# Performance work log

Hardware: AMD Instinct MI355X
Metric: run time of the kernel (lower is better)

The kernel has to match this reference:

```python
import jax, jax.numpy as jnp
import numpy as np

HIDDEN = 2048
KEY_DIM = 2048
NUM_HEADS = 16
EPS = 1e-05


def rms_norm(x, w, eps=EPS):
    ms = jnp.mean(x * x, axis=-1, keepdims=True)
    return x * jax.lax.rsqrt(ms + eps) * w


def setup_inputs() -> dict:
    key = jax.random.key(0)
    ks = jax.random.split(key, 6)
    bound = 1.0 / np.sqrt(HIDDEN)  # kaiming-uniform-ish scale
    x = jax.random.normal(ks[0], (2, 2048, HIDDEN), dtype=jnp.float32)
    rms_w = jnp.ones((HIDDEN,), dtype=jnp.float32)
    Wq = jax.random.uniform(ks[1], (HIDDEN, KEY_DIM), jnp.float32, -bound, bound)
    Wk = jax.random.uniform(ks[2], (HIDDEN, KEY_DIM), jnp.float32, -bound, bound)
    Wv = jax.random.uniform(ks[3], (HIDDEN, KEY_DIM), jnp.float32, -bound, bound)
    Wo = jax.random.uniform(ks[4], (KEY_DIM, HIDDEN), jnp.float32, -bound, bound)
    return {"x": x, "rms_w": rms_w, "Wq": Wq, "Wk": Wk, "Wv": Wv, "Wo": Wo}


def reference(x, rms_w, Wq, Wk, Wv, Wo):
    B, S, _ = x.shape
    residual = x
    xn = rms_norm(x, rms_w)
    # project and split heads: [B,S,H,Dh]
    q = (xn @ Wq).reshape(B, S, NUM_HEADS, KEY_DIM // NUM_HEADS)
    k = (xn @ Wk).reshape(B, S, NUM_HEADS, KEY_DIM // NUM_HEADS)
    v = (xn @ Wv).reshape(B, S, NUM_HEADS, KEY_DIM // NUM_HEADS)
    # NOTE: original scales by 1/sqrt(key_dim), not head_dim — kept faithful
    scale = 1.0 / jnp.sqrt(jnp.float32(KEY_DIM))
    scores = jnp.einsum('bshd,bthd->bhst', q, k) * scale  # [B,H,S,S]
    causal = jnp.tril(jnp.ones((S, S), dtype=bool))
    scores = jnp.where(causal[None, None], scores, -jnp.inf)
    probs = jax.nn.softmax(scores, axis=-1)  # stable max-subtract internally
    out = jnp.einsum('bhst,bthd->bshd', probs, v).reshape(B, S, KEY_DIM)
    return out @ Wo + residual
```

## Files before the change

### kernel.cpp

```cpp
#include <hip/hip_runtime.h>
#include <math.h>

typedef __attribute__((ext_vector_type(8))) short bf16x8;
typedef __attribute__((ext_vector_type(4))) float f32x4;
typedef __attribute__((ext_vector_type(16))) float f32x16;

#define HID 2048
#define SEQ 2048
#define NH  16
#define DH  128
#define QK_SCALE 0.02209708691207961f

__device__ __forceinline__ ushort f2bf(float f) {
  union { float f; unsigned u; } v; v.f = f;
  unsigned r = v.u + 0x7fffu + ((v.u >> 16) & 1u);
  return (ushort)(r >> 16);
}

__device__ __forceinline__ void gload16(const ushort* g, ushort* l) {
  __builtin_amdgcn_global_load_lds((const __attribute__((address_space(1))) void*)g,
                                   (__attribute__((address_space(3))) void*)l,
                                   16, 0, 0);
}

__global__ __launch_bounds__(256) void k_transpose(const float* __restrict__ W,
                                                   ushort* __restrict__ Wt) {
  __shared__ float t[32][33];
  int n0 = blockIdx.x * 32, k0 = blockIdx.y * 32;
  int tx = threadIdx.x, ty = threadIdx.y;
  for (int i = ty; i < 32; i += 8)
    t[i][tx] = W[(size_t)(k0 + i) * HID + n0 + tx];
  __syncthreads();
  for (int i = ty; i < 32; i += 8)
    Wt[(size_t)(n0 + i) * HID + k0 + tx] = f2bf(t[tx][i]);
}

__global__ __launch_bounds__(256) void k_rmsnorm(const float* __restrict__ x,
                                                 const float* __restrict__ w,
                                                 ushort* __restrict__ xn) {
  int row = blockIdx.x;
  const float* xr = x + (size_t)row * HID;
  int base = threadIdx.x * 8;
  float4 a = *(const float4*)(xr + base);
  float4 c = *(const float4*)(xr + base + 4);
  float ss = a.x*a.x + a.y*a.y + a.z*a.z + a.w*a.w
           + c.x*c.x + c.y*c.y + c.z*c.z + c.w*c.w;
  #pragma unroll
  for (int off = 32; off > 0; off >>= 1) ss += __shfl_xor(ss, off);
  __shared__ float red[4];
  if ((threadIdx.x & 63) == 0) red[threadIdx.x >> 6] = ss;
  __syncthreads();
  float tot = red[0] + red[1] + red[2] + red[3];
  float sc = rsqrtf(tot * (1.0f / HID) + 1e-5f);
  float4 wa = *(const float4*)(w + base);
  float4 wc = *(const float4*)(w + base + 4);
  ushort h[8];
  h[0] = f2bf(a.x * sc * wa.x); h[1] = f2bf(a.y * sc * wa.y);
  h[2] = f2bf(a.z * sc * wa.z); h[3] = f2bf(a.w * sc * wa.w);
  h[4] = f2bf(c.x * sc * wc.x); h[5] = f2bf(c.y * sc * wc.y);
  h[6] = f2bf(c.z * sc * wc.z); h[7] = f2bf(c.w * sc * wc.w);
  int4 pk;
  pk.x = h[0] | ((int)h[1] << 16);
  pk.y = h[2] | ((int)h[3] << 16);
  pk.z = h[4] | ((int)h[5] << 16);
  pk.w = h[6] | ((int)h[7] << 16);
  *(int4*)&xn[(size_t)row * HID + base] = pk;
}

template <int MODE>
__global__ __launch_bounds__(256) void k_gemm(const ushort* __restrict__ A,
                                              const ushort* __restrict__ Bt,
                                              ushort* __restrict__ obf,
                                              ushort* __restrict__ vt,
                                              float* __restrict__ ofl,
                                              const float* __restrict__ resid,
                                              int K) {
  __shared__ ushort sA[128 * 64];
  __shared__ ushort sB[128 * 64];
  const int tid = threadIdx.x;
  const int lane = tid & 63, w = tid >> 6;
  const int wr = w >> 1, wc = w & 1;
  const int bm = blockIdx.y, bn = blockIdx.x;
  const int g = lane >> 4, l15 = lane & 15;
  f32x4 zero = {0.f, 0.f, 0.f, 0.f};
  f32x4 acc[4][4];
  #pragma unroll
  for (int i = 0; i < 4; ++i)
    #pragma unroll
    for (int j = 0; j < 4; ++j) acc[i][j] = zero;

  for (int k0 = 0; k0 < K; k0 += 64) {
    #pragma unroll
    for (int c = 0; c < 4; ++c) {
      int id = (w * 4 + c) * 64 + lane;
      int r = id >> 3, ck = id & 7;
      int ke = k0 + ((ck ^ (r & 7)) * 8);
      gload16(&A[(size_t)(bm * 128 + r) * K + ke], ((ushort*)sA) + (size_t)(w * 4 + c) * 512);
      gload16(&Bt[(size_t)(bn * 128 + r) * K + ke], ((ushort*)sB) + (size_t)(w * 4 + c) * 512);
    }
    __syncthreads();
    #pragma unroll
    for (int kk = 0; kk < 2; ++kk) {
      bf16x8 aF[4], bF[4];
      #pragma unroll
      for (int i = 0; i < 4; ++i) {
        int row = wr * 64 + i * 16 + l15;
        int cp = (kk * 4 + g) ^ (lane & 7);
        aF[i] = *(const bf16x8*)&sA[row * 64 + cp * 8];
      }
      #pragma unroll
      for (int j = 0; j < 4; ++j) {
        int row = wc * 64 + j * 16 + l15;
        int cp = (kk * 4 + g) ^ (lane & 7);
        bF[j] = *(const bf16x8*)&sB[row * 64 + cp * 8];
      }
      #pragma unroll
      for (int i = 0; i < 4; ++i)
        #pragma unroll
        for (int j = 0; j < 4; ++j)
          acc[i][j] = __builtin_amdgcn_mfma_f32_16x16x32_bf16(aF[i], bF[j], acc[i][j], 0, 0, 0);
    }
    __syncthreads();
  }

  int rbase = bm * 128 + wr * 64 + (lane >> 4) * 4;
  int cbase = bn * 128 + wc * 64 + l15;
  #pragma unroll
  for (int i = 0; i < 4; ++i) {
    #pragma unroll
    for (int j = 0; j < 4; ++j) {
      int col = cbase + j * 16;
      #pragma unroll
      for (int r = 0; r < 4; ++r) {
        int row = rbase + i * 16 + r;
        float v = acc[i][j][r];
        if (MODE == 0) {
          ushort hv = f2bf(v);
          if (col < 4096) {
            obf[(size_t)row * 4096 + col] = hv;
          } else {
            int nv = col - 4096;
            int h = nv >> 7, d = nv & 127;
            int b = row >> 11, s = row & 2047;
            vt[(size_t)((b * NH + h) * DH + d) * SEQ + s] = hv;
          }
        } else {
          ofl[(size_t)row * HID + col] = v + resid[(size_t)row * HID + col];
        }
      }
    }
  }
}

__global__ __launch_bounds__(256, 2) void k_attn2(const ushort* __restrict__ qk,
                                                  const ushort* __restrict__ vt,
                                                  ushort* __restrict__ aout) {
  __shared__ ushort sK[64 * 128];
  __shared__ ushort sV[128 * 64];
  const int tid = threadIdx.x;
  const int lane = tid & 63, w = tid >> 6;
  const int h2 = lane >> 5;
  const int l31 = lane & 31;
  const int bid = blockIdx.x;
  const int t = bid >> 3;
  const int bh = (bid & 7) + 8 * (t >> 4);
  const int qblk = 15 - (t & 15);
  const int b = bh >> 4, hh = bh & 15;
  const int q0w = qblk * 128 + w * 32;

  bf16x8 qf[8];
  {
    const ushort* qbase = qk + (size_t)(b * SEQ + q0w + l31) * 4096 + hh * DH;
    #pragma unroll
    for (int kk = 0; kk < 8; ++kk) qf[kk] = *(const bf16x8*)&qbase[kk * 16 + h2 * 8];
  }

  f32x16 accO[4];
  #pragma unroll
  for (int i = 0; i < 4; ++i)
    #pragma unroll
    for (int r = 0; r < 16; ++r) accO[i][r] = 0.f;
  float m_r = -1e30f, l_r = 0.f;

  const int ntile = 2 * qblk + 2;
  for (int tt = 0; tt < ntile; ++tt) {
    const int t0 = tt * 64;
    #pragma unroll
    for (int c = 0; c < 4; ++c) {
      int id = (w * 4 + c) * 64 + lane;
      int kr = id >> 4, ck = id & 15;
      gload16(qk + (size_t)(b * SEQ + t0 + kr) * 4096 + 2048 + hh * DH + ((ck ^ (kr & 7)) * 8),
              ((ushort*)sK) + (size_t)(w * 4 + c) * 512);
      int dr = id >> 3, cv = id & 7;
      gload16(vt + (size_t)(bh * DH + dr) * SEQ + t0 + ((cv ^ (dr & 7)) * 8),
              ((ushort*)sV) + (size_t)(w * 4 + c) * 512);
    }
    __syncthreads();

    if (t0 <= q0w + 31) {
      f32x16 accS[2];
      #pragma unroll
      for (int i = 0; i < 2; ++i)
        #pragma unroll
        for (int r = 0; r < 16; ++r) accS[i][r] = 0.f;
      #pragma unroll
      for (int kt = 0; kt < 2; ++kt) {
        const int row = kt * 32 + l31;
        #pragma unroll
        for (int kk = 0; kk < 8; ++kk) {
          const int cp = (kk * 2 + h2) ^ (lane & 7);
          bf16x8 kf = *(const bf16x8*)&sK[row * 128 + cp * 8];
          accS[kt] = __builtin_amdgcn_mfma_f32_32x32x16_bf16(kf, qf[kk], accS[kt], 0, 0, 0);
        }
      }
      const int qa = q0w + l31;
      float pmax = -INFINITY;
      if (t0 + 63 <= q0w) {
        #pragma unroll
        for (int kt = 0; kt < 2; ++kt)
          #pragma unroll
          for (int r = 0; r < 16; ++r) {
            float s = accS[kt][r] * QK_SCALE;
            accS[kt][r] = s;
            pmax = fmaxf(pmax, s);
          }
      } else {
        #pragma unroll
        for (int kt = 0; kt < 2; ++kt)
          #pragma unroll
          for (int r = 0; r < 16; ++r) {
            int ka = t0 + kt * 32 + (r & 3) + 8 * (r >> 2) + 4 * h2;
            float s = (ka <= qa) ? accS[kt][r] * QK_SCALE : -INFINITY;
            accS[kt][r] = s;
            pmax = fmaxf(pmax, s);
          }
      }
      pmax = fmaxf(pmax, __shfl_xor(pmax, 32));
      if (__any(pmax > m_r + 8.f)) {
        float mn = fmaxf(m_r, pmax);
        float al = __expf(m_r - mn);
        m_r = mn;
        l_r *= al;
        #pragma unroll
        for (int r = 0; r < 16; ++r) {
          float ar = __shfl(al, (r & 3) + 8 * (r >> 2) + 4 * h2);
          #pragma unroll
          for (int ds = 0; ds < 4; ++ds) accO[ds][r] *= ar;
        }
      }
      float rs = 0.f;
      #pragma unroll
      for (int kt = 0; kt < 2; ++kt)
        #pragma unroll
        for (int r = 0; r < 16; ++r) {
          float p = __expf(accS[kt][r] - m_r);
          rs += p;
          accS[kt][r] = p;
        }
      rs += __shfl_xor(rs, 32);
      l_r += rs;
      uint W[2][4][2];
      #pragma unroll
      for (int kt = 0; kt < 2; ++kt)
        #pragma unroll
        for (int bq = 0; bq < 4; ++bq)
          #pragma unroll
          for (int w2 = 0; w2 < 2; ++w2) {
            uint u0 = __float_as_uint(accS[kt][bq * 4 + w2 * 2]);
            uint u1 = __float_as_uint(accS[kt][bq * 4 + w2 * 2 + 1]);
            W[kt][bq][w2] = (u0 >> 16) | (u1 & 0xffff0000u);
          }
      #pragma unroll
      for (int kc = 0; kc < 4; ++kc) {
        const int kt = kc >> 1, pq = kc & 1;
        uint X0 = W[kt][2 * pq][0],     X1 = W[kt][2 * pq][1];
        uint Y0 = W[kt][2 * pq + 1][0], Y1 = W[kt][2 * pq + 1][1];
        uint sx0 = (uint)__shfl_xor((int)X0, 32);
        uint sx1 = (uint)__shfl_xor((int)X1, 32);
        uint sy0 = (uint)__shfl_xor((int)Y0, 32);
        uint sy1 = (uint)__shfl_xor((int)Y1, 32);
        union { uint u[4]; bf16x8 v; } pu;
        pu.u[0] = h2 ? sy0 : X0;
        pu.u[1] = h2 ? sy1 : X1;
        pu.u[2] = h2 ? Y0 : sx0;
        pu.u[3] = h2 ? Y1 : sx1;
        #pragma unroll
        for (int ds = 0; ds < 4; ++ds) {
          const int dr = ds * 32 + l31;
          const int cp = (kc * 2 + h2) ^ (lane & 7);
          bf16x8 vf = *(const bf16x8*)&sV[dr * 64 + cp * 8];
          accO[ds] = __builtin_amdgcn_mfma_f32_32x32x16_bf16(pu.v, vf, accO[ds], 0, 0, 0);
        }
      }
    }
    __syncthreads();
  }

  float linv = 1.f / l_r;
  #pragma unroll
  for (int r = 0; r < 16; ++r) {
    int qrel = (r & 3) + 8 * (r >> 2) + 4 * h2;
    float li = __shfl(linv, qrel);
    #pragma unroll
    for (int ds = 0; ds < 4; ++ds) {
      aout[(size_t)(b * SEQ + q0w + qrel) * HID + hh * DH + ds * 32 + l31] =
          f2bf(accO[ds][r] * li);
    }
  }
}

extern "C" void kernel_launch(void* const* d_in, const int* in_sizes, int n_in,
                              void* d_out, int out_size, void* d_ws, size_t ws_size,
                              hipStream_t stream) {
  const float* x     = (const float*)d_in[0];
  const float* rms_w = (const float*)d_in[1];
  const float* Wq    = (const float*)d_in[2];
  const float* Wk    = (const float*)d_in[3];
  const float* Wv    = (const float*)d_in[4];
  const float* Wo    = (const float*)d_in[5];
  float* out = (float*)d_out;

  char* ws = (char*)d_ws;
  ushort* WqkvT = (ushort*)ws; ws += (size_t)6144 * 2048 * 2;
  ushort* WoT   = (ushort*)ws; ws += (size_t)2048 * 2048 * 2;
  ushort* xn    = (ushort*)ws; ws += (size_t)4096 * 2048 * 2;
  ushort* qkbuf = (ushort*)ws; ws += (size_t)4096 * 4096 * 2;
  ushort* vt    = (ushort*)ws; ws += (size_t)4096 * 2048 * 2;
  ushort* aout  = (ushort*)ws; ws += (size_t)4096 * 2048 * 2;

  dim3 tb(32, 8), tg(64, 64);
  k_transpose<<<tg, tb, 0, stream>>>(Wq, WqkvT);
  k_transpose<<<tg, tb, 0, stream>>>(Wk, WqkvT + (size_t)2048 * 2048);
  k_transpose<<<tg, tb, 0, stream>>>(Wv, WqkvT + (size_t)4096 * 2048);
  k_transpose<<<tg, tb, 0, stream>>>(Wo, WoT);

  k_rmsnorm<<<4096, 256, 0, stream>>>(x, rms_w, xn);

  k_gemm<0><<<dim3(48, 32), 256, 0, stream>>>(xn, WqkvT, qkbuf, vt, nullptr, nullptr, 2048);

  k_attn2<<<512, 256, 0, stream>>>(qkbuf, vt, aout);

  k_gemm<1><<<dim3(16, 32), 256, 0, stream>>>(aout, WoT, nullptr, nullptr, out, x, 2048);
}
```

Measured before the change: 302.0 us.

## Rewrite GEMM with 256x128 tiles, 4-stage async LDS pipeline and block swizzle

Replaces the single-buffered 128x128 GEMM with a 512-thread 256x128-tile kernel. It uses a 4-deep ring of LDS buffers filled by direct global-to-LDS loads, with vmcnt-based waits so loads overlap MFMA compute, and raises wave priority around the MFMA block. Block indices are swizzled so that consecutive blocks share operand tiles, aimed at better cache reuse. The changes are meant to hide global load latency and remove the double __syncthreads per k-step, at the cost of more LDS (96KB) and hand-tuned waitcnt logic that relies on exact load counts.

New measurement: 293.3 us. 1.03x faster.

```diff
diff --git a/kernel.cpp b/kernel.cpp
--- a/kernel.cpp
+++ b/kernel.cpp
@@ -68,63 +68,96 @@
 }
 
 template <int MODE>
-__global__ __launch_bounds__(256) void k_gemm(const ushort* __restrict__ A,
-                                              const ushort* __restrict__ Bt,
-                                              ushort* __restrict__ obf,
-                                              ushort* __restrict__ vt,
-                                              float* __restrict__ ofl,
-                                              const float* __restrict__ resid,
-                                              int K) {
-  __shared__ ushort sA[128 * 64];
-  __shared__ ushort sB[128 * 64];
+__global__ __launch_bounds__(512, 2) void k_gemm2(const ushort* __restrict__ A,
+                                                  const ushort* __restrict__ Bt,
+                                                  ushort* __restrict__ obf,
+                                                  ushort* __restrict__ vt,
+                                                  float* __restrict__ ofl,
+                                                  const float* __restrict__ resid) {
+  constexpr int K = 2048, NS = 64;
+  constexpr int NBN = (MODE == 0) ? 48 : 16;
+  constexpr int QX = ((MODE == 0) ? 768 : 256) / 8;
+  __shared__ ushort lds[4][12288];
   const int tid = threadIdx.x;
   const int lane = tid & 63, w = tid >> 6;
-  const int wr = w >> 1, wc = w & 1;
-  const int bm = blockIdx.y, bn = blockIdx.x;
+  const int wm = w >> 1, wn = w & 1;
   const int g = lane >> 4, l15 = lane & 15;
-  f32x4 zero = {0.f, 0.f, 0.f, 0.f};
+  const int swz = (blockIdx.x & 7) * QX + (blockIdx.x >> 3);
+  const int bm = swz / NBN, bn = swz % NBN;
+
   f32x4 acc[4][4];
   #pragma unroll
   for (int i = 0; i < 4; ++i)
     #pragma unroll
-    for (int j = 0; j < 4; ++j) acc[i][j] = zero;
-
-  for (int k0 = 0; k0 < K; k0 += 64) {
-    #pragma unroll
-    for (int c = 0; c < 4; ++c) {
-      int id = (w * 4 + c) * 64 + lane;
-      int r = id >> 3, ck = id & 7;
-      int ke = k0 + ((ck ^ (r & 7)) * 8);
-      gload16(&A[(size_t)(bm * 128 + r) * K + ke], ((ushort*)sA) + (size_t)(w * 4 + c) * 512);
-      gload16(&Bt[(size_t)(bn * 128 + r) * K + ke], ((ushort*)sB) + (size_t)(w * 4 + c) * 512);
-    }
-    __syncthreads();
-    #pragma unroll
-    for (int kk = 0; kk < 2; ++kk) {
-      bf16x8 aF[4], bF[4];
-      #pragma unroll
-      for (int i = 0; i < 4; ++i) {
-        int row = wr * 64 + i * 16 + l15;
-        int cp = (kk * 4 + g) ^ (lane & 7);
-        aF[i] = *(const bf16x8*)&sA[row * 64 + cp * 8];
-      }
-      #pragma unroll
-      for (int j = 0; j < 4; ++j) {
-        int row = wc * 64 + j * 16 + l15;
-        int cp = (kk * 4 + g) ^ (lane & 7);
-        bF[j] = *(const bf16x8*)&sB[row * 64 + cp * 8];
-      }
-      #pragma unroll
-      for (int i = 0; i < 4; ++i)
-        #pragma unroll
-        for (int j = 0; j < 4; ++j)
-          acc[i][j] = __builtin_amdgcn_mfma_f32_16x16x32_bf16(aF[i], bF[j], acc[i][j], 0, 0, 0);
-    }
-    __syncthreads();
-  }
-
-  int rbase = bm * 128 + wr * 64 + (lane >> 4) * 4;
-  int cbase = bn * 128 + wc * 64 + l15;
+    for (int j = 0; j < 4; ++j) acc[i][j] = f32x4{0.f, 0.f, 0.f, 0.f};
+
+  auto STAGE = [&](int s) {
+    const int ch = s & 3, k0 = s * 32;
+    #pragma unroll
+    for (int c = 0; c < 2; ++c) {
+      int idx = c * 512 + tid;
+      int r = idx >> 2, cp = idx & 3;
+      int ck = cp ^ ((r >> 1) & 3);
+      gload16(&A[(size_t)(bm * 256 + r) * K + k0 + ck * 8],
+              &lds[ch][(c * 8 + w) * 512]);
+    }
+    {
+      int r = tid >> 2, cp = tid & 3;
+      int ck = cp ^ ((r >> 1) & 3);
+      gload16(&Bt[(size_t)(bn * 128 + r) * K + k0 + ck * 8],
+              &lds[ch][8192 + w * 512]);
+    }
+  };
+
+  auto COMPUTE = [&](int s) {
+    const ushort* La = lds[s & 3];
+    const ushort* Lb = La + 8192;
+    bf16x8 aF[4], bF[4];
+    #pragma unroll
+    for (int i = 0; i < 4; ++i) {
+      int row = wm * 64 + i * 16 + l15;
+      int cp = g ^ ((row >> 1) & 3);
+      aF[i] = *(const bf16x8*)&La[row * 32 + cp * 8];
+    }
+    #pragma unroll
+    for (int j = 0; j < 4; ++j) {
+      int row = wn * 64 + j * 16 + l15;
+      int cp = g ^ ((row >> 1) & 3);
+      bF[j] = *(const bf16x8*)&Lb[row * 32 + cp * 8];
+    }
+    __builtin_amdgcn_s_setprio(1);
+    #pragma unroll
+    for (int i = 0; i < 4; ++i)
+      #pragma unroll
+      for (int j = 0; j < 4; ++j)
+        acc[i][j] = __builtin_amdgcn_mfma_f32_16x16x32_bf16(aF[i], bF[j], acc[i][j], 0, 0, 0);
+    __builtin_amdgcn_s_setprio(0);
+  };
+
+  STAGE(0); STAGE(1); STAGE(2);
+  #pragma unroll 1
+  for (int s = 0; s <= NS - 4; ++s) {
+    asm volatile("s_waitcnt vmcnt(6)" ::: "memory");
+    __builtin_amdgcn_s_barrier();
+    __builtin_amdgcn_sched_barrier(0);
+    STAGE(s + 3);
+    COMPUTE(s);
+  }
+  asm volatile("s_waitcnt vmcnt(6)" ::: "memory");
+  __builtin_amdgcn_s_barrier();
+  __builtin_amdgcn_sched_barrier(0);
+  COMPUTE(NS - 3);
+  asm volatile("s_waitcnt vmcnt(3)" ::: "memory");
+  __builtin_amdgcn_s_barrier();
+  __builtin_amdgcn_sched_barrier(0);
+  COMPUTE(NS - 2);
+  asm volatile("s_waitcnt vmcnt(0)" ::: "memory");
+  __builtin_amdgcn_s_barrier();
+  __builtin_amdgcn_sched_barrier(0);
+  COMPUTE(NS - 1);
+
+  int rbase = bm * 256 + wm * 64 + g * 4;
+  int cbase = bn * 128 + wn * 64 + l15;
   #pragma unroll
   for (int i = 0; i < 4; ++i) {
     #pragma unroll
@@ -336,9 +369,9 @@
 
   k_rmsnorm<<<4096, 256, 0, stream>>>(x, rms_w, xn);
 
-  k_gemm<0><<<dim3(48, 32), 256, 0, stream>>>(xn, WqkvT, qkbuf, vt, nullptr, nullptr, 2048);
+  k_gemm2<0><<<768, 512, 0, stream>>>(xn, WqkvT, qkbuf, vt, nullptr, nullptr);
 
   k_attn2<<<512, 256, 0, stream>>>(qkbuf, vt, aout);
 
-  k_gemm<1><<<dim3(16, 32), 256, 0, stream>>>(aout, WoT, nullptr, nullptr, out, x, 2048);
-}
+  k_gemm2<1><<<256, 512, 0, stream>>>(aout, WoT, nullptr, nullptr, out, x);
+}
```

## Double-buffer LDS in GEMM and attention loops, merge weight transposes into one launch

Applied to the files above, without the earlier changes.

The GEMM and attention kernels now double-buffer their shared-memory tiles and prefetch the next tile with async global-to-LDS loads while computing the current one. Explicit vmcnt waits and raw barriers replace __syncthreads, so memory latency can overlap MFMA work. The four weight-transpose launches are merged into one 3D-grid launch. Shared memory per block doubles, which may lower occupancy, especially for the attention kernel with its launch bound of 2 blocks.

Measured after the change: 301.8 us. Within noise of the previous version (-0.1%).

```diff
diff --git a/kernel.cpp b/kernel.cpp
--- a/kernel.cpp
+++ b/kernel.cpp
@@ -23,9 +23,19 @@
                                    16, 0, 0);
 }
 
-__global__ __launch_bounds__(256) void k_transpose(const float* __restrict__ W,
-                                                   ushort* __restrict__ Wt) {
+#define VMCNT(n) asm volatile("s_waitcnt vmcnt(" #n ")" ::: "memory")
+#define BAR()    __builtin_amdgcn_s_barrier()
+
+__global__ __launch_bounds__(256) void k_transpose4(const float* __restrict__ W0,
+                                                    const float* __restrict__ W1,
+                                                    const float* __restrict__ W2,
+                                                    const float* __restrict__ W3,
+                                                    ushort* __restrict__ T0,
+                                                    ushort* __restrict__ T3) {
   __shared__ float t[32][33];
+  int z = blockIdx.z;
+  const float* W = (z == 0) ? W0 : (z == 1) ? W1 : (z == 2) ? W2 : W3;
+  ushort* Wt = (z == 3) ? T3 : (T0 + (size_t)z * 2048 * 2048);
   int n0 = blockIdx.x * 32, k0 = blockIdx.y * 32;
   int tx = threadIdx.x, ty = threadIdx.y;
   for (int i = ty; i < 32; i += 8)
@@ -68,37 +78,38 @@
 }
 
 template <int MODE>
-__global__ __launch_bounds__(256) void k_gemm(const ushort* __restrict__ A,
-                                              const ushort* __restrict__ Bt,
-                                              ushort* __restrict__ obf,
-                                              ushort* __restrict__ vt,
-                                              float* __restrict__ ofl,
-                                              const float* __restrict__ resid,
-                                              int K) {
-  __shared__ ushort sA[128 * 64];
-  __shared__ ushort sB[128 * 64];
+__global__ __launch_bounds__(256) void k_gemm4(const ushort* __restrict__ A,
+                                               const ushort* __restrict__ Bt,
+                                               ushort* __restrict__ obf,
+                                               ushort* __restrict__ vt,
+                                               float* __restrict__ ofl,
+                                               const float* __restrict__ resid,
+                                               int K) {
+  __shared__ ushort sA[2][128 * 64];
+  __shared__ ushort sB[2][128 * 64];
   const int tid = threadIdx.x;
   const int lane = tid & 63, w = tid >> 6;
   const int wr = w >> 1, wc = w & 1;
   const int bm = blockIdx.y, bn = blockIdx.x;
   const int g = lane >> 4, l15 = lane & 15;
-  f32x4 zero = {0.f, 0.f, 0.f, 0.f};
   f32x4 acc[4][4];
   #pragma unroll
   for (int i = 0; i < 4; ++i)
     #pragma unroll
-    for (int j = 0; j < 4; ++j) acc[i][j] = zero;
-
-  for (int k0 = 0; k0 < K; k0 += 64) {
+    for (int j = 0; j < 4; ++j) acc[i][j] = f32x4{0.f, 0.f, 0.f, 0.f};
+
+  auto STAGE = [&](int t, int buf) {
+    const int k0 = t * 64;
     #pragma unroll
     for (int c = 0; c < 4; ++c) {
       int id = (w * 4 + c) * 64 + lane;
       int r = id >> 3, ck = id & 7;
       int ke = k0 + ((ck ^ (r & 7)) * 8);
-      gload16(&A[(size_t)(bm * 128 + r) * K + ke], ((ushort*)sA) + (size_t)(w * 4 + c) * 512);
-      gload16(&Bt[(size_t)(bn * 128 + r) * K + ke], ((ushort*)sB) + (size_t)(w * 4 + c) * 512);
-    }
-    __syncthreads();
+      gload16(&A[(size_t)(bm * 128 + r) * K + ke], &sA[buf][(w * 4 + c) * 512]);
+      gload16(&Bt[(size_t)(bn * 128 + r) * K + ke], &sB[buf][(w * 4 + c) * 512]);
+    }
+  };
+  auto COMPUTE = [&](int buf) {
     #pragma unroll
     for (int kk = 0; kk < 2; ++kk) {
       bf16x8 aF[4], bF[4];
@@ -106,13 +117,13 @@
       for (int i = 0; i < 4; ++i) {
         int row = wr * 64 + i * 16 + l15;
         int cp = (kk * 4 + g) ^ (lane & 7);
-        aF[i] = *(const bf16x8*)&sA[row * 64 + cp * 8];
+        aF[i] = *(const bf16x8*)&sA[buf][row * 64 + cp * 8];
       }
       #pragma unroll
       for (int j = 0; j < 4; ++j) {
         int row = wc * 64 + j * 16 + l15;
         int cp = (kk * 4 + g) ^ (lane & 7);
-        bF[j] = *(const bf16x8*)&sB[row * 64 + cp * 8];
+        bF[j] = *(const bf16x8*)&sB[buf][row * 64 + cp * 8];
       }
       #pragma unroll
       for (int i = 0; i < 4; ++i)
@@ -120,10 +131,23 @@
         for (int j = 0; j < 4; ++j)
           acc[i][j] = __builtin_amdgcn_mfma_f32_16x16x32_bf16(aF[i], bF[j], acc[i][j], 0, 0, 0);
     }
-    __syncthreads();
-  }
-
-  int rbase = bm * 128 + wr * 64 + (lane >> 4) * 4;
+  };
+
+  const int nt = K / 64;
+  STAGE(0, 0);
+  #pragma unroll 1
+  for (int t = 0; t < nt - 1; ++t) {
+    STAGE(t + 1, (t + 1) & 1);
+    VMCNT(8);
+    BAR();
+    COMPUTE(t & 1);
+    BAR();
+  }
+  VMCNT(0);
+  BAR();
+  COMPUTE((nt - 1) & 1);
+
+  int rbase = bm * 128 + wr * 64 + g * 4;
   int cbase = bn * 128 + wc * 64 + l15;
   #pragma unroll
   for (int i = 0; i < 4; ++i) {
@@ -152,11 +176,11 @@
   }
 }
 
-__global__ __launch_bounds__(256, 2) void k_attn2(const ushort* __restrict__ qk,
+__global__ __launch_bounds__(256, 2) void k_attn3(const ushort* __restrict__ qk,
                                                   const ushort* __restrict__ vt,
                                                   ushort* __restrict__ aout) {
-  __shared__ ushort sK[64 * 128];
-  __shared__ ushort sV[128 * 64];
+  __shared__ ushort sK[2][64 * 128];
+  __shared__ ushort sV[2][128 * 64];
   const int tid = threadIdx.x;
   const int lane = tid & 63, w = tid >> 6;
   const int h2 = lane >> 5;
@@ -182,119 +206,131 @@
     for (int r = 0; r < 16; ++r) accO[i][r] = 0.f;
   float m_r = -1e30f, l_r = 0.f;
 
-  const int ntile = 2 * qblk + 2;
-  for (int tt = 0; tt < ntile; ++tt) {
+  auto STAGE = [&](int tt, int buf) {
     const int t0 = tt * 64;
     #pragma unroll
     for (int c = 0; c < 4; ++c) {
       int id = (w * 4 + c) * 64 + lane;
       int kr = id >> 4, ck = id & 15;
       gload16(qk + (size_t)(b * SEQ + t0 + kr) * 4096 + 2048 + hh * DH + ((ck ^ (kr & 7)) * 8),
-              ((ushort*)sK) + (size_t)(w * 4 + c) * 512);
+              &sK[buf][(size_t)(w * 4 + c) * 512]);
       int dr = id >> 3, cv = id & 7;
       gload16(vt + (size_t)(bh * DH + dr) * SEQ + t0 + ((cv ^ (dr & 7)) * 8),
-              ((ushort*)sV) + (size_t)(w * 4 + c) * 512);
-    }
-    __syncthreads();
-
-    if (t0 <= q0w + 31) {
-      f32x16 accS[2];
-      #pragma unroll
-      for (int i = 0; i < 2; ++i)
-        #pragma unroll
-        for (int r = 0; r < 16; ++r) accS[i][r] = 0.f;
-      #pragma unroll
-      for (int kt = 0; kt < 2; ++kt) {
-        const int row = kt * 32 + l31;
-        #pragma unroll
-        for (int kk = 0; kk < 8; ++kk) {
-          const int cp = (kk * 2 + h2) ^ (lane & 7);
-          bf16x8 kf = *(const bf16x8*)&sK[row * 128 + cp * 8];
-          accS[kt] = __builtin_amdgcn_mfma_f32_32x32x16_bf16(kf, qf[kk], accS[kt], 0, 0, 0);
+              &sV[buf][(size_t)(w * 4 + c) * 512]);
+    }
+  };
+
+  auto COMPUTE = [&](int tt, int buf) {
+    const int t0 = tt * 64;
+    f32x16 accS[2];
+    #pragma unroll
+    for (int i = 0; i < 2; ++i)
+      #pragma unroll
+      for (int r = 0; r < 16; ++r) accS[i][r] = 0.f;
+    #pragma unroll
+    for (int kt = 0; kt < 2; ++kt) {
+      const int row = kt * 32 + l31;
+      #pragma unroll
+      for (int kk = 0; kk < 8; ++kk) {
+        const int cp = (kk * 2 + h2) ^ (lane & 7);
+        bf16x8 kf = *(const bf16x8*)&sK[buf][row * 128 + cp * 8];
+        accS[kt] = __builtin_amdgcn_mfma_f32_32x32x16_bf16(kf, qf[kk], accS[kt], 0, 0, 0);
+      }
+    }
+    const int qa = q0w + l31;
+    float pmax = -INFINITY;
+    if (t0 + 63 <= q0w) {
+      #pragma unroll
+      for (int kt = 0; kt < 2; ++kt)
+        #pragma unroll
+        for (int r = 0; r < 16; ++r) {
+          float s = accS[kt][r] * QK_SCALE;
+          accS[kt][r] = s;
+          pmax = fmaxf(pmax, s);
         }
-      }
-      const int qa = q0w + l31;
-      float pmax = -INFINITY;
-      if (t0 + 63 <= q0w) {
-        #pragma unroll
-        for (int kt = 0; kt < 2; ++kt)
-          #pragma unroll
-          for (int r = 0; r < 16; ++r) {
-            float s = accS[kt][r] * QK_SCALE;
-            accS[kt][r] = s;
-            pmax = fmaxf(pmax, s);
-          }
-      } else {
-        #pragma unroll
-        for (int kt = 0; kt < 2; ++kt)
-          #pragma unroll
-          for (int r = 0; r < 16; ++r) {
-            int ka = t0 + kt * 32 + (r & 3) + 8 * (r >> 2) + 4 * h2;
-            float s = (ka <= qa) ? accS[kt][r] * QK_SCALE : -INFINITY;
-            accS[kt][r] = s;
-            pmax = fmaxf(pmax, s);
-          }
-      }
-      pmax = fmaxf(pmax, __shfl_xor(pmax, 32));
-      if (__any(pmax > m_r + 8.f)) {
-        float mn = fmaxf(m_r, pmax);
-        float al = __expf(m_r - mn);
-        m_r = mn;
-        l_r *= al;
+    } else {
+      #pragma unroll
+      for (int kt = 0; kt < 2; ++kt)
         #pragma unroll
         for (int r = 0; r < 16; ++r) {
-          float ar = __shfl(al, (r & 3) + 8 * (r >> 2) + 4 * h2);
-          #pragma unroll
-          for (int ds = 0; ds < 4; ++ds) accO[ds][r] *= ar;
+          int ka = t0 + kt * 32 + (r & 3) + 8 * (r >> 2) + 4 * h2;
+          float s = (ka <= qa) ? accS[kt][r] * QK_SCALE : -INFINITY;
+          accS[kt][r] = s;
+          pmax = fmaxf(pmax, s);
         }
-      }
-      float rs = 0.f;
-      #pragma unroll
-      for (int kt = 0; kt < 2; ++kt)
-        #pragma unroll
-        for (int r = 0; r < 16; ++r) {
-          float p = __expf(accS[kt][r] - m_r);
-          rs += p;
-          accS[kt][r] = p;
+    }
+    pmax = fmaxf(pmax, __shfl_xor(pmax, 32));
+    if (__any(pmax > m_r + 8.f)) {
+      float mn = fmaxf(m_r, pmax);
+      float al = __expf(m_r - mn);
+      m_r = mn;
+      l_r *= al;
+      #pragma unroll
+      for (int r = 0; r < 16; ++r) {
+        float ar = __shfl(al, (r & 3) + 8 * (r >> 2) + 4 * h2);
+        #pragma unroll
+        for (int ds = 0; ds < 4; ++ds) accO[ds][r] *= ar;
+      }
+    }
+    float rs = 0.f;
+    #pragma unroll
+    for (int kt = 0; kt < 2; ++kt)
+      #pragma unroll
+      for (int r = 0; r < 16; ++r) {
+        float p = __expf(accS[kt][r] - m_r);
+        rs += p;
+        accS[kt][r] = p;
+      }
+    rs += __shfl_xor(rs, 32);
+    l_r += rs;
+    uint W[2][4][2];
+    #pragma unroll
+    for (int kt = 0; kt < 2; ++kt)
+      #pragma unroll
+      for (int bq = 0; bq < 4; ++bq)
+        #pragma unroll
+        for (int w2 = 0; w2 < 2; ++w2) {
+          uint u0 = __float_as_uint(accS[kt][bq * 4 + w2 * 2]);
+          uint u1 = __float_as_uint(accS[kt][bq * 4 + w2 * 2 + 1]);
+          W[kt][bq][w2] = (u0 >> 16) | (u1 & 0xffff0000u);
         }
-      rs += __shfl_xor(rs, 32);
-      l_r += rs;
-      uint W[2][4][2];
-      #pragma unroll
-      for (int kt = 0; kt < 2; ++kt)
-        #pragma unroll
-        for (int bq = 0; bq < 4; ++bq)
-          #pragma unroll
-          for (int w2 = 0; w2 < 2; ++w2) {
-            uint u0 = __float_as_uint(accS[kt][bq * 4 + w2 * 2]);
-            uint u1 = __float_as_uint(accS[kt][bq * 4 + w2 * 2 + 1]);
-            W[kt][bq][w2] = (u0 >> 16) | (u1 & 0xffff0000u);
-          }
-      #pragma unroll
-      for (int kc = 0; kc < 4; ++kc) {
-        const int kt = kc >> 1, pq = kc & 1;
-        uint X0 = W[kt][2 * pq][0],     X1 = W[kt][2 * pq][1];
-        uint Y0 = W[kt][2 * pq + 1][0], Y1 = W[kt][2 * pq + 1][1];
-        uint sx0 = (uint)__shfl_xor((int)X0, 32);
-        uint sx1 = (uint)__shfl_xor((int)X1, 32);
-        uint sy0 = (uint)__shfl_xor((int)Y0, 32);
-        uint sy1 = (uint)__shfl_xor((int)Y1, 32);
-        union { uint u[4]; bf16x8 v; } pu;
-        pu.u[0] = h2 ? sy0 : X0;
-        pu.u[1] = h2 ? sy1 : X1;
-        pu.u[2] = h2 ? Y0 : sx0;
-        pu.u[3] = h2 ? Y1 : sx1;
-        #pragma unroll
-        for (int ds = 0; ds < 4; ++ds) {
-          const int dr = ds * 32 + l31;
-          const int cp = (kc * 2 + h2) ^ (lane & 7);
-          bf16x8 vf = *(const bf16x8*)&sV[dr * 64 + cp * 8];
-          accO[ds] = __builtin_amdgcn_mfma_f32_32x32x16_bf16(pu.v, vf, accO[ds], 0, 0, 0);
-        }
-      }
-    }
-    __syncthreads();
-  }
+    #pragma unroll
+    for (int kc = 0; kc < 4; ++kc) {
+      const int kt = kc >> 1, pq = kc & 1;
+      uint X0 = W[kt][2 * pq][0],     X1 = W[kt][2 * pq][1];
+      uint Y0 = W[kt][2 * pq + 1][0], Y1 = W[kt][2 * pq + 1][1];
+      uint sx0 = (uint)__shfl_xor((int)X0, 32);
+      uint sx1 = (uint)__shfl_xor((int)X1, 32);
+      uint sy0 = (uint)__shfl_xor((int)Y0, 32);
+      uint sy1 = (uint)__shfl_xor((int)Y1, 32);
+      union { uint u[4]; bf16x8 v; } pu;
+      pu.u[0] = h2 ? sy0 : X0;
+      pu.u[1] = h2 ? sy1 : X1;
+      pu.u[2] = h2 ? Y0 : sx0;
+      pu.u[3] = h2 ? Y1 : sx1;
+      #pragma unroll
+      for (int ds = 0; ds < 4; ++ds) {
+        const int dr = ds * 32 + l31;
+        const int cp = (kc * 2 + h2) ^ (lane & 7);
+        bf16x8 vf = *(const bf16x8*)&sV[buf][dr * 64 + cp * 8];
+        accO[ds] = __builtin_amdgcn_mfma_f32_32x32x16_bf16(pu.v, vf, accO[ds], 0, 0, 0);
+      }
+    }
+  };
+
+  const int ntile = 2 * qblk + 2;
+  STAGE(0, 0);
+  #pragma unroll 1
+  for (int tt = 0; tt < ntile - 1; ++tt) {
+    STAGE(tt + 1, (tt + 1) & 1);
+    VMCNT(8);
+    BAR();
+    if (tt * 64 <= q0w + 31) COMPUTE(tt, tt & 1);
+    BAR();
+  }
+  VMCNT(0);
+  BAR();
+  COMPUTE(ntile - 1, (ntile - 1) & 1);
 
   float linv = 1.f / l_r;
   #pragma unroll
@@ -328,17 +364,13 @@
   ushort* vt    = (ushort*)ws; ws += (size_t)4096 * 2048 * 2;
   ushort* aout  = (ushort*)ws; ws += (size_t)4096 * 2048 * 2;
 
-  dim3 tb(32, 8), tg(64, 64);
-  k_transpose<<<tg, tb, 0, stream>>>(Wq, WqkvT);
-  k_transpose<<<tg, tb, 0, stream>>>(Wk, WqkvT + (size_t)2048 * 2048);
-  k_transpose<<<tg, tb, 0, stream>>>(Wv, WqkvT + (size_t)4096 * 2048);
-  k_transpose<<<tg, tb, 0, stream>>>(Wo, WoT);
+  k_transpose4<<<dim3(64, 64, 4), dim3(32, 8), 0, stream>>>(Wq, Wk, Wv, Wo, WqkvT, WoT);
 
   k_rmsnorm<<<4096, 256, 0, stream>>>(x, rms_w, xn);
 
-  k_gemm<0><<<dim3(48, 32), 256, 0, stream>>>(xn, WqkvT, qkbuf, vt, nullptr, nullptr, 2048);
-
-  k_attn2<<<512, 256, 0, stream>>>(qkbuf, vt, aout);
-
-  k_gemm<1><<<dim3(16, 32), 256, 0, stream>>>(aout, WoT, nullptr, nullptr, out, x, 2048);
-}
+  k_gemm4<0><<<dim3(48, 32), 256, 0, stream>>>(xn, WqkvT, qkbuf, vt, nullptr, nullptr, 2048);
+
+  k_attn3<<<512, 256, 0, stream>>>(qkbuf, vt, aout);
+
+  k_gemm4<1><<<dim3(16, 32), 256, 0, stream>>>(aout, WoT, nullptr, nullptr, out, x, 2048);
+}
```

## Enlarge GEMM tiles to 256x128 and merge four weight transposes into one launch

Applied to the files above, without the earlier changes.

The GEMM block tile grows from 128x128 to 256x128, so each wave now computes a 128x64 sub-tile with 8x4 MFMA accumulators. This raises arithmetic intensity per LDS load and halves the number of blocks. The four separate weight-transpose launches are folded into a single 3D-grid launch to cut launch overhead. The cost is more registers per thread and more LDS per block. The output-projection GEMM shrinks to only 256 blocks, which may underfill the 256 CUs.

After: 311.0 us. 3.0% more time.

```diff
diff --git a/kernel.cpp b/kernel.cpp
--- a/kernel.cpp
+++ b/kernel.cpp
@@ -23,9 +23,16 @@
                                    16, 0, 0);
 }
 
-__global__ __launch_bounds__(256) void k_transpose(const float* __restrict__ W,
-                                                   ushort* __restrict__ Wt) {
+__global__ __launch_bounds__(256) void k_transpose4(const float* __restrict__ W0,
+                                                    const float* __restrict__ W1,
+                                                    const float* __restrict__ W2,
+                                                    const float* __restrict__ W3,
+                                                    ushort* __restrict__ T0,
+                                                    ushort* __restrict__ T3) {
   __shared__ float t[32][33];
+  int z = blockIdx.z;
+  const float* W = (z == 0) ? W0 : (z == 1) ? W1 : (z == 2) ? W2 : W3;
+  ushort* Wt = (z == 3) ? T3 : (T0 + (size_t)z * 2048 * 2048);
   int n0 = blockIdx.x * 32, k0 = blockIdx.y * 32;
   int tx = threadIdx.x, ty = threadIdx.y;
   for (int i = ty; i < 32; i += 8)
@@ -68,43 +75,48 @@
 }
 
 template <int MODE>
-__global__ __launch_bounds__(256) void k_gemm(const ushort* __restrict__ A,
-                                              const ushort* __restrict__ Bt,
-                                              ushort* __restrict__ obf,
-                                              ushort* __restrict__ vt,
-                                              float* __restrict__ ofl,
-                                              const float* __restrict__ resid,
-                                              int K) {
-  __shared__ ushort sA[128 * 64];
+__global__ __launch_bounds__(256, 2) void k_gemm6(const ushort* __restrict__ A,
+                                                  const ushort* __restrict__ Bt,
+                                                  ushort* __restrict__ obf,
+                                                  ushort* __restrict__ vt,
+                                                  float* __restrict__ ofl,
+                                                  const float* __restrict__ resid,
+                                                  int K) {
+  __shared__ ushort sA[256 * 64];
   __shared__ ushort sB[128 * 64];
   const int tid = threadIdx.x;
   const int lane = tid & 63, w = tid >> 6;
   const int wr = w >> 1, wc = w & 1;
   const int bm = blockIdx.y, bn = blockIdx.x;
   const int g = lane >> 4, l15 = lane & 15;
-  f32x4 zero = {0.f, 0.f, 0.f, 0.f};
-  f32x4 acc[4][4];
-  #pragma unroll
-  for (int i = 0; i < 4; ++i)
-    #pragma unroll
-    for (int j = 0; j < 4; ++j) acc[i][j] = zero;
+  f32x4 acc[8][4];
+  #pragma unroll
+  for (int i = 0; i < 8; ++i)
+    #pragma unroll
+    for (int j = 0; j < 4; ++j) acc[i][j] = f32x4{0.f, 0.f, 0.f, 0.f};
 
   for (int k0 = 0; k0 < K; k0 += 64) {
+    #pragma unroll
+    for (int c = 0; c < 8; ++c) {
+      int id = (w * 8 + c) * 64 + lane;
+      int r = id >> 3, ck = id & 7;
+      gload16(&A[(size_t)(bm * 256 + r) * K + k0 + ((ck ^ (r & 7)) * 8)],
+              ((ushort*)sA) + (size_t)(w * 8 + c) * 512);
+    }
     #pragma unroll
     for (int c = 0; c < 4; ++c) {
       int id = (w * 4 + c) * 64 + lane;
       int r = id >> 3, ck = id & 7;
-      int ke = k0 + ((ck ^ (r & 7)) * 8);
-      gload16(&A[(size_t)(bm * 128 + r) * K + ke], ((ushort*)sA) + (size_t)(w * 4 + c) * 512);
-      gload16(&Bt[(size_t)(bn * 128 + r) * K + ke], ((ushort*)sB) + (size_t)(w * 4 + c) * 512);
+      gload16(&Bt[(size_t)(bn * 128 + r) * K + k0 + ((ck ^ (r & 7)) * 8)],
+              ((ushort*)sB) + (size_t)(w * 4 + c) * 512);
     }
     __syncthreads();
     #pragma unroll
     for (int kk = 0; kk < 2; ++kk) {
-      bf16x8 aF[4], bF[4];
-      #pragma unroll
-      for (int i = 0; i < 4; ++i) {
-        int row = wr * 64 + i * 16 + l15;
+      bf16x8 aF[8], bF[4];
+      #pragma unroll
+      for (int i = 0; i < 8; ++i) {
+        int row = wr * 128 + i * 16 + l15;
         int cp = (kk * 4 + g) ^ (lane & 7);
         aF[i] = *(const bf16x8*)&sA[row * 64 + cp * 8];
       }
@@ -115,7 +127,7 @@
         bF[j] = *(const bf16x8*)&sB[row * 64 + cp * 8];
       }
       #pragma unroll
-      for (int i = 0; i < 4; ++i)
+      for (int i = 0; i < 8; ++i)
         #pragma unroll
         for (int j = 0; j < 4; ++j)
           acc[i][j] = __builtin_amdgcn_mfma_f32_16x16x32_bf16(aF[i], bF[j], acc[i][j], 0, 0, 0);
@@ -123,10 +135,10 @@
     __syncthreads();
   }
 
-  int rbase = bm * 128 + wr * 64 + (lane >> 4) * 4;
+  int rbase = bm * 256 + wr * 128 + g * 4;
   int cbase = bn * 128 + wc * 64 + l15;
   #pragma unroll
-  for (int i = 0; i < 4; ++i) {
+  for (int i = 0; i < 8; ++i) {
     #pragma unroll
     for (int j = 0; j < 4; ++j) {
       int col = cbase + j * 16;
@@ -328,17 +340,13 @@
   ushort* vt    = (ushort*)ws; ws += (size_t)4096 * 2048 * 2;
   ushort* aout  = (ushort*)ws; ws += (size_t)4096 * 2048 * 2;
 
-  dim3 tb(32, 8), tg(64, 64);
-  k_transpose<<<tg, tb, 0, stream>>>(Wq, WqkvT);
-  k_transpose<<<tg, tb, 0, stream>>>(Wk, WqkvT + (size_t)2048 * 2048);
-  k_transpose<<<tg, tb, 0, stream>>>(Wv, WqkvT + (size_t)4096 * 2048);
-  k_transpose<<<tg, tb, 0, stream>>>(Wo, WoT);
+  k_transpose4<<<dim3(64, 64, 4), dim3(32, 8), 0, stream>>>(Wq, Wk, Wv, Wo, WqkvT, WoT);
 
   k_rmsnorm<<<4096, 256, 0, stream>>>(x, rms_w, xn);
 
-  k_gemm<0><<<dim3(48, 32), 256, 0, stream>>>(xn, WqkvT, qkbuf, vt, nullptr, nullptr, 2048);
+  k_gemm6<0><<<dim3(48, 16), 256, 0, stream>>>(xn, WqkvT, qkbuf, vt, nullptr, nullptr, 2048);
 
   k_attn2<<<512, 256, 0, stream>>>(qkbuf, vt, aout);
 
-  k_gemm<1><<<dim3(16, 32), 256, 0, stream>>>(aout, WoT, nullptr, nullptr, out, x, 2048);
-}
+  k_gemm6<1><<<dim3(16, 16), 256, 0, stream>>>(aout, WoT, nullptr, nullptr, out, x, 2048);
+}
```
